# Optimization experiments

Measured on AMD Instinct MI355X. Metric: run time of the kernel, lower is better.

Reference implementation:

```python
import jax, jax.numpy as jnp
import numpy as np

B, T, D, H = 32, 4096, 512, 512


def setup_inputs() -> dict:
    key = jax.random.key(0)
    ks = jax.random.split(key, 8)
    s = 1.0 / np.sqrt(D)
    return {
        "hidden_state": jax.random.normal(ks[0], (B, D), jnp.float32),
        "encoder_outputs": jax.random.normal(ks[1], (B, T, D), jnp.float32),
        "W": jax.random.normal(ks[2], (D, H), jnp.float32) * s,
        "U": jax.random.normal(ks[3], (D, H), jnp.float32) * s,
        "V": jax.random.normal(ks[4], (H,), jnp.float32) * s,
        "bias": jnp.zeros((H,), jnp.float32),
        "Wa": jax.random.normal(ks[5], (H, H), jnp.float32) * (1.0 / np.sqrt(H)),
        "ba": jnp.zeros((H,), jnp.float32),
    }


def reference(hidden_state, encoder_outputs, W, U, V, bias, Wa, ba):
    # dens1: [B,1,H] ; dens2: [B,T,H]
    dens1 = jnp.einsum('bd,dh->bh', hidden_state, W)[:, None, :]
    dens2 = jnp.einsum('btd,dh->bth', encoder_outputs, U)
    pre = dens1 + dens2 + bias                       # [B,T,H]
    tanh_ = jnp.tanh(jnp.einsum('bth,hk->btk', pre, Wa) + ba)  # extra Dense(tanh)
    cij = jnp.einsum('bth,h->bt', tanh_, V)          # [B,T]
    alphas = jax.nn.softmax(cij, axis=-1)            # [B,T]
    output = jnp.einsum('btd,bt->bd', encoder_outputs, alphas)  # weighted sum
    return output, alphas
```

## Files before the change

kernel.cpp:

```cpp
#include <hip/hip_runtime.h>
#include <hip/hip_bf16.h>


#define BB 32
#define TT 4096
#define DD 512
#define HH 512
#define MM (BB * TT)

typedef short s16x8 __attribute__((ext_vector_type(8)));
typedef float f32x4 __attribute__((ext_vector_type(4)));

union FU { float f; unsigned u; };

static __device__ __forceinline__ unsigned pack_bf16_trunc(float a, float b) {
    FU ua, ub; ua.f = a; ub.f = b;
    return (ua.u >> 16) | (ub.u & 0xffff0000u);
}

static __device__ __forceinline__ unsigned short f2bf_rne(float x) {
    FU v; v.f = x;
    unsigned u = v.u;
    u = u + 0x7fffu + ((u >> 16) & 1u);
    return (unsigned short)(u >> 16);
}

static __device__ __forceinline__ float tanh_fast(float x) {
    float e = __expf(2.0f * x);
    return 1.0f - 2.0f * __builtin_amdgcn_rcpf(e + 1.0f);
}

__global__ void k_dens1(const float* __restrict__ hs, const float* __restrict__ W,
                        const float* __restrict__ bias, float* __restrict__ g) {
    int bi = blockIdx.x;
    int dc = bi & 3, hb = (bi >> 2) & 1, b = bi >> 3;
    int h = hb * 256 + threadIdx.x;
    float s = (dc == 0) ? bias[h] : 0.0f;
    int d0 = dc * 128;
    #pragma unroll 4
    for (int d = 0; d < 128; ++d)
        s = fmaf(hs[b * DD + d0 + d], W[(size_t)(d0 + d) * HH + h], s);
    atomicAdd(&g[b * HH + h], s);
}

__global__ void k_cvec(const float* __restrict__ g, const float* __restrict__ Wa,
                       const float* __restrict__ ba, float* __restrict__ cvec) {
    int bi = blockIdx.x;
    int hc = bi & 3, kb = (bi >> 2) & 1, b = bi >> 3;
    int k = kb * 256 + threadIdx.x;
    float s = (hc == 0) ? ba[k] : 0.0f;
    int h0 = hc * 128;
    #pragma unroll 4
    for (int h = 0; h < 128; ++h)
        s = fmaf(g[b * HH + h0 + h], Wa[(size_t)(h0 + h) * HH + k], s);
    atomicAdd(&cvec[b * HH + k], s);
}

__global__ void k_uwa(const float* __restrict__ U, const float* __restrict__ Wa,
                      unsigned short* __restrict__ UWaT) {
    int d0 = blockIdx.x * 4;
    int tid = threadIdx.x;
    __shared__ float Us[4][DD];
    #pragma unroll
    for (int i = 0; i < 8; ++i) {
        int idx = i * 256 + tid;
        Us[idx >> 9][idx & 511] = U[(size_t)(d0 + (idx >> 9)) * HH + (idx & 511)];
    }
    __syncthreads();
    float acc[4][2] = {};
    #pragma unroll 4
    for (int h = 0; h < DD; ++h) {
        float w0 = Wa[(size_t)h * HH + tid];
        float w1 = Wa[(size_t)h * HH + 256 + tid];
        #pragma unroll
        for (int dd = 0; dd < 4; ++dd) {
            float u = Us[dd][h];
            acc[dd][0] = fmaf(u, w0, acc[dd][0]);
            acc[dd][1] = fmaf(u, w1, acc[dd][1]);
        }
    }
    #pragma unroll
    for (int dd = 0; dd < 4; ++dd) {
        UWaT[(size_t)tid * DD + d0 + dd] = f2bf_rne(acc[dd][0]);
        UWaT[(size_t)(tid + 256) * DD + d0 + dd] = f2bf_rne(acc[dd][1]);
    }
}

#define LDA 72

__global__ void __launch_bounds__(256) k_gemm_tanh(
    const float* __restrict__ e, const unsigned short* __restrict__ Bt,
    const float* __restrict__ cvec, const float* __restrict__ V,
    float* __restrict__ cij) {
    int tid = threadIdx.x;
    int n_tile = blockIdx.x & 3;
    int m_tile = blockIdx.x >> 2;
    int m0 = m_tile << 7;
    int n0 = n_tile << 7;
    int lane = tid & 63, wid = tid >> 6;
    int wm = (wid >> 1) << 6;
    int wn = (wid & 1) << 6;
    int lcol = lane & 15, q = lane >> 4;

    __shared__ __align__(16) unsigned short As[128 * LDA];
    __shared__ __align__(16) unsigned short Bs[128 * LDA];

    f32x4 acc[4][4] = {};

    const float* Abase = e + (size_t)m0 * DD;
    const unsigned short* Bbase = Bt + (size_t)n0 * DD;

    for (int k0 = 0; k0 < DD; k0 += 64) {
        #pragma unroll
        for (int it = 0; it < 8; ++it) {
            int idx = it * 256 + tid;
            int row = idx >> 4, c4 = idx & 15;
            float4 v = *(const float4*)(Abase + (size_t)row * DD + k0 + c4 * 4);
            uint2 w;
            w.x = pack_bf16_trunc(v.x, v.y);
            w.y = pack_bf16_trunc(v.z, v.w);
            *(uint2*)&As[row * LDA + c4 * 4] = w;
        }
        #pragma unroll
        for (int it = 0; it < 4; ++it) {
            int idx = it * 256 + tid;
            int row = idx >> 3, c8 = idx & 7;
            int4 v = *(const int4*)(Bbase + (size_t)row * DD + k0 + c8 * 8);
            *(int4*)&Bs[row * LDA + c8 * 8] = v;
        }
        __syncthreads();
        #pragma unroll
        for (int ks = 0; ks < 64; ks += 32) {
            s16x8 af[4], bfr[4];
            #pragma unroll
            for (int i = 0; i < 4; ++i)
                af[i] = *(const s16x8*)&As[(wm + i * 16 + lcol) * LDA + ks + q * 8];
            #pragma unroll
            for (int j = 0; j < 4; ++j)
                bfr[j] = *(const s16x8*)&Bs[(wn + j * 16 + lcol) * LDA + ks + q * 8];
            #pragma unroll
            for (int i = 0; i < 4; ++i)
                #pragma unroll
                for (int j = 0; j < 4; ++j)
                    acc[i][j] = __builtin_amdgcn_mfma_f32_16x16x32_bf16(
                        af[i], bfr[j], acc[i][j], 0, 0, 0);
        }
        __syncthreads();
    }

    int b = m0 >> 12;
    float cvv[4], Vv[4];
    #pragma unroll
    for (int j = 0; j < 4; ++j) {
        int h = n0 + wn + j * 16 + lcol;
        cvv[j] = cvec[b * HH + h];
        Vv[j] = V[h];
    }
    #pragma unroll
    for (int i = 0; i < 4; ++i) {
        #pragma unroll
        for (int r = 0; r < 4; ++r) {
            float s = 0.0f;
            #pragma unroll
            for (int j = 0; j < 4; ++j) {
                float pre = acc[i][j][r] + cvv[j];
                s = fmaf(tanh_fast(pre), Vv[j], s);
            }
            s += __shfl_xor(s, 1);
            s += __shfl_xor(s, 2);
            s += __shfl_xor(s, 4);
            s += __shfl_xor(s, 8);
            if (lcol == 0)
                atomicAdd(&cij[m0 + wm + i * 16 + q * 4 + r], s);
        }
    }
}

__global__ void k_softmax(const float* __restrict__ cij, float* __restrict__ alphas) {
    int b = blockIdx.x, tid = threadIdx.x;
    const float* row = cij + (size_t)b * TT;
    __shared__ float red[4];
    float m = -1e30f;
    for (int t = tid; t < TT; t += 256) m = fmaxf(m, row[t]);
    #pragma unroll
    for (int o = 1; o < 64; o <<= 1) m = fmaxf(m, __shfl_xor(m, o));
    if ((tid & 63) == 0) red[tid >> 6] = m;
    __syncthreads();
    m = fmaxf(fmaxf(red[0], red[1]), fmaxf(red[2], red[3]));
    __syncthreads();
    float sum = 0.0f;
    for (int t = tid; t < TT; t += 256) sum += __expf(row[t] - m);
    #pragma unroll
    for (int o = 1; o < 64; o <<= 1) sum += __shfl_xor(sum, o);
    if ((tid & 63) == 0) red[tid >> 6] = sum;
    __syncthreads();
    float inv = 1.0f / (red[0] + red[1] + red[2] + red[3]);
    for (int t = tid; t < TT; t += 256)
        alphas[(size_t)b * TT + t] = __expf(row[t] - m) * inv;
}

__global__ void k_wsum(const float* __restrict__ e, const float* __restrict__ alphas,
                       float* __restrict__ out) {
    int b = blockIdx.x >> 5;
    int t0 = (blockIdx.x & 31) * 128;
    int tid = threadIdx.x;
    int half = tid >> 7, f4 = tid & 127;
    const float* base = e + (size_t)b * TT * DD;
    float4 acc = {0.0f, 0.0f, 0.0f, 0.0f};
    for (int it = 0; it < 64; ++it) {
        int t = t0 + it * 2 + half;
        float a = alphas[(size_t)b * TT + t];
        float4 v = *(const float4*)(base + (size_t)t * DD + f4 * 4);
        acc.x = fmaf(a, v.x, acc.x);
        acc.y = fmaf(a, v.y, acc.y);
        acc.z = fmaf(a, v.z, acc.z);
        acc.w = fmaf(a, v.w, acc.w);
    }
    float* o = out + b * DD + f4 * 4;
    atomicAdd(o + 0, acc.x);
    atomicAdd(o + 1, acc.y);
    atomicAdd(o + 2, acc.z);
    atomicAdd(o + 3, acc.w);
}

extern "C" void kernel_launch(void* const* d_in, const int* in_sizes, int n_in,
                              void* d_out, int out_size, void* d_ws, size_t ws_size,
                              hipStream_t stream) {
    const float* hs   = (const float*)d_in[0];
    const float* e    = (const float*)d_in[1];
    const float* W    = (const float*)d_in[2];
    const float* U    = (const float*)d_in[3];
    const float* V    = (const float*)d_in[4];
    const float* bias = (const float*)d_in[5];
    const float* Wa   = (const float*)d_in[6];
    const float* ba   = (const float*)d_in[7];

    float* out    = (float*)d_out;
    float* alphas = out + BB * DD;

    float*          cij  = (float*)d_ws;
    float*          g    = (float*)((char*)d_ws + 524288);
    float*          cvec = (float*)((char*)d_ws + 589824);
    unsigned short* Bt   = (unsigned short*)((char*)d_ws + 655360);

    hipMemsetAsync(d_ws, 0, 655360, stream);
    hipMemsetAsync(d_out, 0, BB * DD * sizeof(float), stream);

    k_dens1<<<256, 256, 0, stream>>>(hs, W, bias, g);
    k_cvec<<<256, 256, 0, stream>>>(g, Wa, ba, cvec);
    k_uwa<<<128, 256, 0, stream>>>(U, Wa, Bt);
    k_gemm_tanh<<<4096, 256, 0, stream>>>(e, Bt, cvec, V, cij);
    k_softmax<<<BB, 256, 0, stream>>>(cij, alphas);
    k_wsum<<<BB * 32, 256, 0, stream>>>(e, alphas, out);
}
```

Measured before the change: 603.0 us.

## Retile tanh GEMM to full-N 64-row tiles with direct-to-LDS B loads

The fused GEMM+tanh kernel now has each block cover 64 rows across the whole 512-wide N dimension, instead of a 128x128 tile. Each encoder row is therefore read and converted to bf16 once rather than four times. B tiles are loaded with global_load_lds directly into LDS, and the A tile uses an XOR-swizzled layout to avoid bank conflicts. The weighted-sum kernel is split into more, smaller blocks with two independent accumulators. The risk is lower occupancy from 32 accumulator tiles per wave and a 64KB B tile in LDS.

```diff
diff --git a/kernel.cpp b/kernel.cpp
--- a/kernel.cpp
+++ b/kernel.cpp
@@ -6,7 +6,7 @@
 #define TT 4096
 #define DD 512
 #define HH 512
-#define MM (BB * TT)
+#define BK 64
 
 typedef short s16x8 __attribute__((ext_vector_type(8)));
 typedef float f32x4 __attribute__((ext_vector_type(4)));
@@ -28,6 +28,12 @@
 static __device__ __forceinline__ float tanh_fast(float x) {
     float e = __expf(2.0f * x);
     return 1.0f - 2.0f * __builtin_amdgcn_rcpf(e + 1.0f);
+}
+
+static __device__ __forceinline__ void gload_lds16(const void* g, void* l) {
+    __builtin_amdgcn_global_load_lds(
+        (const __attribute__((address_space(1))) unsigned int*)g,
+        (__attribute__((address_space(3))) unsigned int*)l, 16, 0, 0);
 }
 
 __global__ void k_dens1(const float* __restrict__ hs, const float* __restrict__ W,
@@ -86,62 +92,59 @@
     }
 }
 
-#define LDA 72
-
-__global__ void __launch_bounds__(256) k_gemm_tanh(
+__global__ void __launch_bounds__(256, 2) k_gemm_tanh(
     const float* __restrict__ e, const unsigned short* __restrict__ Bt,
     const float* __restrict__ cvec, const float* __restrict__ V,
     float* __restrict__ cij) {
     int tid = threadIdx.x;
-    int n_tile = blockIdx.x & 3;
-    int m_tile = blockIdx.x >> 2;
-    int m0 = m_tile << 7;
-    int n0 = n_tile << 7;
-    int lane = tid & 63, wid = tid >> 6;
-    int wm = (wid >> 1) << 6;
-    int wn = (wid & 1) << 6;
+    int m0 = blockIdx.x * 64;
+    int lane = tid & 63, w = tid >> 6;
+    int wn = w * 128;
     int lcol = lane & 15, q = lane >> 4;
 
-    __shared__ __align__(16) unsigned short As[128 * LDA];
-    __shared__ __align__(16) unsigned short Bs[128 * LDA];
-
-    f32x4 acc[4][4] = {};
+    __shared__ __align__(16) unsigned short As[64 * BK];
+    __shared__ __align__(16) unsigned short Bs[512 * BK];
+
+    f32x4 acc[4][8] = {};
 
     const float* Abase = e + (size_t)m0 * DD;
-    const unsigned short* Bbase = Bt + (size_t)n0 * DD;
-
-    for (int k0 = 0; k0 < DD; k0 += 64) {
-        #pragma unroll
-        for (int it = 0; it < 8; ++it) {
+
+    for (int k0 = 0; k0 < DD; k0 += BK) {
+        #pragma unroll
+        for (int u = 0; u < 16; ++u) {
+            int p = w * 16 + u;
+            int g = p >> 3, c0 = (p & 7) * 64;
+            const unsigned short* gp = Bt + (size_t)(c0 + lane) * DD + k0 + g * 8;
+            gload_lds16(gp, &Bs[(g * 512 + c0) * 8]);
+        }
+        #pragma unroll
+        for (int it = 0; it < 4; ++it) {
             int idx = it * 256 + tid;
             int row = idx >> 4, c4 = idx & 15;
             float4 v = *(const float4*)(Abase + (size_t)row * DD + k0 + c4 * 4);
-            uint2 w;
-            w.x = pack_bf16_trunc(v.x, v.y);
-            w.y = pack_bf16_trunc(v.z, v.w);
-            *(uint2*)&As[row * LDA + c4 * 4] = w;
-        }
-        #pragma unroll
-        for (int it = 0; it < 4; ++it) {
-            int idx = it * 256 + tid;
-            int row = idx >> 3, c8 = idx & 7;
-            int4 v = *(const int4*)(Bbase + (size_t)row * DD + k0 + c8 * 8);
-            *(int4*)&Bs[row * LDA + c8 * 8] = v;
+            uint2 wv;
+            wv.x = pack_bf16_trunc(v.x, v.y);
+            wv.y = pack_bf16_trunc(v.z, v.w);
+            int g = c4 >> 1, half = c4 & 1;
+            *(uint2*)&As[(g * 64 + (row ^ g)) * 8 + half * 4] = wv;
         }
         __syncthreads();
         #pragma unroll
-        for (int ks = 0; ks < 64; ks += 32) {
-            s16x8 af[4], bfr[4];
-            #pragma unroll
-            for (int i = 0; i < 4; ++i)
-                af[i] = *(const s16x8*)&As[(wm + i * 16 + lcol) * LDA + ks + q * 8];
-            #pragma unroll
-            for (int j = 0; j < 4; ++j)
-                bfr[j] = *(const s16x8*)&Bs[(wn + j * 16 + lcol) * LDA + ks + q * 8];
+        for (int ks = 0; ks < BK; ks += 32) {
+            int gk = ks >> 3;
+            s16x8 af[4], bfr[8];
+            #pragma unroll
+            for (int i = 0; i < 4; ++i) {
+                int row = i * 16 + lcol, g = gk + q;
+                af[i] = *(const s16x8*)&As[(g * 64 + (row ^ g)) * 8];
+            }
+            #pragma unroll
+            for (int j = 0; j < 8; ++j)
+                bfr[j] = *(const s16x8*)&Bs[((gk + q) * 512 + wn + j * 16 + lcol) * 8];
             #pragma unroll
             for (int i = 0; i < 4; ++i)
                 #pragma unroll
-                for (int j = 0; j < 4; ++j)
+                for (int j = 0; j < 8; ++j)
                     acc[i][j] = __builtin_amdgcn_mfma_f32_16x16x32_bf16(
                         af[i], bfr[j], acc[i][j], 0, 0, 0);
         }
@@ -149,10 +152,10 @@
     }
 
     int b = m0 >> 12;
-    float cvv[4], Vv[4];
-    #pragma unroll
-    for (int j = 0; j < 4; ++j) {
-        int h = n0 + wn + j * 16 + lcol;
+    float cvv[8], Vv[8];
+    #pragma unroll
+    for (int j = 0; j < 8; ++j) {
+        int h = wn + j * 16 + lcol;
         cvv[j] = cvec[b * HH + h];
         Vv[j] = V[h];
     }
@@ -162,16 +165,14 @@
         for (int r = 0; r < 4; ++r) {
             float s = 0.0f;
             #pragma unroll
-            for (int j = 0; j < 4; ++j) {
-                float pre = acc[i][j][r] + cvv[j];
-                s = fmaf(tanh_fast(pre), Vv[j], s);
-            }
+            for (int j = 0; j < 8; ++j)
+                s = fmaf(tanh_fast(acc[i][j][r] + cvv[j]), Vv[j], s);
             s += __shfl_xor(s, 1);
             s += __shfl_xor(s, 2);
             s += __shfl_xor(s, 4);
             s += __shfl_xor(s, 8);
             if (lcol == 0)
-                atomicAdd(&cij[m0 + wm + i * 16 + q * 4 + r], s);
+                atomicAdd(&cij[m0 + i * 16 + q * 4 + r], s);
         }
     }
 }
@@ -201,26 +202,27 @@
 
 __global__ void k_wsum(const float* __restrict__ e, const float* __restrict__ alphas,
                        float* __restrict__ out) {
-    int b = blockIdx.x >> 5;
-    int t0 = (blockIdx.x & 31) * 128;
+    int b = blockIdx.x >> 6;
+    int t0 = (blockIdx.x & 63) * 64;
     int tid = threadIdx.x;
     int half = tid >> 7, f4 = tid & 127;
     const float* base = e + (size_t)b * TT * DD;
-    float4 acc = {0.0f, 0.0f, 0.0f, 0.0f};
-    for (int it = 0; it < 64; ++it) {
-        int t = t0 + it * 2 + half;
-        float a = alphas[(size_t)b * TT + t];
-        float4 v = *(const float4*)(base + (size_t)t * DD + f4 * 4);
-        acc.x = fmaf(a, v.x, acc.x);
-        acc.y = fmaf(a, v.y, acc.y);
-        acc.z = fmaf(a, v.z, acc.z);
-        acc.w = fmaf(a, v.w, acc.w);
-    }
+    const float* al = alphas + (size_t)b * TT;
+    f32x4 a0 = {0, 0, 0, 0}, a1 = {0, 0, 0, 0};
+    for (int it = 0; it < 16; ++it) {
+        int t = t0 + it * 4 + half;
+        float w0 = al[t], w1 = al[t + 2];
+        f32x4 v0 = *(const f32x4*)(base + (size_t)t * DD + f4 * 4);
+        f32x4 v1 = *(const f32x4*)(base + (size_t)(t + 2) * DD + f4 * 4);
+        a0 += w0 * v0;
+        a1 += w1 * v1;
+    }
+    a0 += a1;
     float* o = out + b * DD + f4 * 4;
-    atomicAdd(o + 0, acc.x);
-    atomicAdd(o + 1, acc.y);
-    atomicAdd(o + 2, acc.z);
-    atomicAdd(o + 3, acc.w);
+    atomicAdd(o + 0, a0[0]);
+    atomicAdd(o + 1, a0[1]);
+    atomicAdd(o + 2, a0[2]);
+    atomicAdd(o + 3, a0[3]);
 }
 
 extern "C" void kernel_launch(void* const* d_in, const int* in_sizes, int n_in,
@@ -249,7 +251,7 @@
     k_dens1<<<256, 256, 0, stream>>>(hs, W, bias, g);
     k_cvec<<<256, 256, 0, stream>>>(g, Wa, ba, cvec);
     k_uwa<<<128, 256, 0, stream>>>(U, Wa, Bt);
-    k_gemm_tanh<<<4096, 256, 0, stream>>>(e, Bt, cvec, V, cij);
+    k_gemm_tanh<<<2048, 256, 0, stream>>>(e, Bt, cvec, V, cij);
     k_softmax<<<BB, 256, 0, stream>>>(cij, alphas);
-    k_wsum<<<BB * 32, 256, 0, stream>>>(e, alphas, out);
-}
+    k_wsum<<<BB * 64, 256, 0, stream>>>(e, alphas, out);
+}
```

New measurement: 629.8 us. 4.5% more time.
